# Optimization experiments

Measured on AMD Instinct MI355X. Metric: run time of the kernel, lower is better.

## Reference

```python
import jax, jax.numpy as jnp
import numpy as np

N_ATOMS = 16384
APC = 64            # atoms per conformer
N_CONF = 256        # 64 mols * 4 confs
N_MOL = 64
DEG = 32
E = N_ATOMS * DEG
H = 128             # hidden_channels = num_filters = out_channels
G = 50              # num_gaussians
L = 6               # num_interactions
CUTOFF = 10.0
LOG2 = float(np.log(2.0))


def ssp(x):
    # ShiftedSoftplus: softplus(x) - log(2)
    return jax.nn.softplus(x) - LOG2


def setup_inputs() -> dict:
    key = jax.random.key(0)
    ks = jax.random.split(key, 24)
    rng = np.random.default_rng(0)

    z = jnp.asarray(rng.integers(1, 100, size=(N_ATOMS,)), dtype=jnp.int64 if jax.config.jax_enable_x64 else jnp.int32)
    # positions uniform in a 5A box -> all intra-conformer distances < cutoff
    pos = jax.random.uniform(ks[0], (N_ATOMS, 3), dtype=jnp.float32) * 5.0

    # within-conformer random edges, no self loops (radius_graph surrogate)
    i = np.repeat(np.arange(N_ATOMS), DEG)
    off = rng.integers(1, APC, size=E)
    j = (i // APC) * APC + (i % APC + off) % APC
    edge_index = jnp.asarray(np.stack([j, i]), dtype=jnp.int32)  # [2,E] (source, target)

    atom_to_conf = jnp.asarray(np.arange(N_ATOMS) // APC, dtype=jnp.int32)
    conf_to_mol = jnp.asarray(np.arange(N_CONF) // (N_CONF // N_MOL), dtype=jnp.int32)

    s = 0.05
    p = {
        'emb':     jax.random.normal(ks[1], (120, H), jnp.float32) * s,
        # per-interaction stacked params [L, ...]
        'mlp_w1':  jax.random.normal(ks[2], (L, G, H), jnp.float32) * s,
        'mlp_b1':  jnp.zeros((L, H), jnp.float32),
        'mlp_w2':  jax.random.normal(ks[3], (L, H, H), jnp.float32) * s,
        'mlp_b2':  jnp.zeros((L, H), jnp.float32),
        'cf_w1':   jax.random.normal(ks[4], (L, H, H), jnp.float32) * s,
        'cf_w2':   jax.random.normal(ks[5], (L, H, H), jnp.float32) * s,
        'cf_b2':   jnp.zeros((L, H), jnp.float32),
        'int_w':   jax.random.normal(ks[6], (L, H, H), jnp.float32) * s,
        'int_b':   jnp.zeros((L, H), jnp.float32),
        # readout head
        'out_w1':  jax.random.normal(ks[7], (H, H), jnp.float32) * s,
        'out_b1':  jnp.zeros((H,), jnp.float32),
        'out_w2':  jax.random.normal(ks[8], (H, H), jnp.float32) * s,
        'out_b2':  jnp.zeros((H,), jnp.float32),
        'head_w1': jax.random.normal(ks[9], (H, H // 2), jnp.float32) * s,
        'head_b1': jnp.zeros((H // 2,), jnp.float32),
        'head_w2': jax.random.normal(ks[10], (H // 2, 1), jnp.float32) * s,
        'head_b2': jnp.zeros((1,), jnp.float32),
    }
    return dict(z=z, pos=pos, edge_index=edge_index, atom_to_conf=atom_to_conf,
                conf_to_mol=conf_to_mol, **p)


def reference(z, pos, edge_index, atom_to_conf, conf_to_mol, emb,
              mlp_w1, mlp_b1, mlp_w2, mlp_b2, cf_w1, cf_w2, cf_b2,
              int_w, int_b, out_w1, out_b1, out_w2, out_b2,
              head_w1, head_b1, head_w2, head_b2):
    row, col = edge_index[0], edge_index[1]  # message from row, aggregated at col

    h = emb[z]                                             # [N,H]
    edge_weight = jnp.linalg.norm(pos[row] - pos[col], axis=-1)  # [E]

    # GaussianSmearing
    offset = jnp.linspace(0.0, CUTOFF, G)
    coeff = -0.5 / (offset[1] - offset[0]) ** 2
    edge_attr = jnp.exp(coeff * (edge_weight[:, None] - offset[None, :]) ** 2)  # [E,G]

    C = 0.5 * (jnp.cos(edge_weight * jnp.pi / CUTOFF) + 1.0)  # cosine cutoff [E]

    for l in range(L):
        # filter network on edge features, modulated by cutoff envelope
        Wf = ssp(edge_attr @ mlp_w1[l] + mlp_b1[l]) @ mlp_w2[l] + mlp_b2[l]
        Wf = Wf * C[:, None]                               # [E,H]
        xf = h @ cf_w1[l]                                  # lin1 (no bias) [N,H]
        msg = xf[row] * Wf                                 # gather * filter [E,H]
        agg = jax.ops.segment_sum(msg, col, num_segments=N_ATOMS)  # scatter-add [N,H]
        xc = agg @ cf_w2[l] + cf_b2[l]                     # lin2
        h = h + (ssp(xc) @ int_w[l] + int_b[l])            # act, lin, residual

    h = ssp(h @ out_w1 + out_b1)
    h = h @ out_w2 + out_b2                                # [N,H]

    conf_emb = jax.ops.segment_sum(h, atom_to_conf, num_segments=N_CONF)   # [C,H]
    mol_emb = jax.ops.segment_sum(conf_emb, conf_to_mol, num_segments=N_MOL)  # [M,H]

    out = (ssp(mol_emb @ head_w1 + head_b1) @ head_w2 + head_b2)[:, 0]  # [M]
    return out
```

## Files before the change

### kernel.cpp

```cpp
#include <hip/hip_runtime.h>
#include <math.h>

#define N_ATOMS 16384
#define APC 64
#define N_CONF 256
#define N_MOL 64
#define DEG 32
#define NEDGE (N_ATOMS * DEG)
#define H 128
#define G 50
#define NL 6
#define TP0 1024
#define TPB 4096
#define CUTOFF 10.0f

typedef __attribute__((ext_vector_type(8))) short short8_t;
typedef __attribute__((ext_vector_type(4))) float f32x4;

__device__ __forceinline__ float ssp_f(float x) {
  float e = __expf(-fabsf(x));
  return fmaxf(x, 0.f) + __logf(1.f + e) - 0.69314718055994531f;
}
__device__ __forceinline__ unsigned short bf16_rne(float x) {
  unsigned u = __float_as_uint(x);
  unsigned r = u + 0x7FFF + ((u >> 16) & 1);
  return (unsigned short)(r >> 16);
}
__device__ __forceinline__ float bf16_to_f(unsigned short s) {
  return __uint_as_float(((unsigned)s) << 16);
}
__device__ __forceinline__ float bflo(unsigned u) { return __uint_as_float(u << 16); }
__device__ __forceinline__ float bfhi(unsigned u) { return __uint_as_float(u & 0xFFFF0000u); }

__global__ __launch_bounds__(256) void k_setup(
    const float* __restrict__ pos, const int* __restrict__ esrc,
    const int* __restrict__ etgt, int* __restrict__ pk,
    const float* __restrict__ cf_w1, const float* __restrict__ cf_w2,
    const float* __restrict__ int_w, const float* __restrict__ out_w1,
    const float* __restrict__ out_w2, short* __restrict__ PW,
    const float* __restrict__ w1, const float* __restrict__ b1,
    const float* __restrict__ w2, const float* __restrict__ b2,
    float* __restrict__ T) {
  __shared__ float g2[2][64];
  __shared__ float S2[2][128];
  const int b = blockIdx.x;
  const int tid = threadIdx.x;
  if (b < 2048) {
    int e = b * 256 + tid;
    int r = esrc[e], c = etgt[e];
    float dx = pos[r * 3 + 0] - pos[c * 3 + 0];
    float dy = pos[r * 3 + 1] - pos[c * 3 + 1];
    float dz = pos[r * 3 + 2] - pos[c * 3 + 2];
    float d = sqrtf(dx * dx + dy * dy + dz * dz);
    int i = (int)(d * ((float)(TPB - 1) / CUTOFF) + 0.5f);
    if (i > TPB - 1) i = TPB - 1;
    if (i < 0) i = 0;
    pk[e] = i | ((r & (APC - 1)) << 16);
  } else if (b < 2208) {
    int e = (b - 2048) * 256 + tid;
    int g = e >> 11, t = e & 2047;
    int kb = t >> 9, rem = t & 511, nt = rem >> 6, lane = rem & 63;
    int quad = lane >> 4, ln = lane & 15;
    int kbase = kb * 32 + quad * 8;
    int n = nt * 16 + ln;
    const float* src;
    if (g < 12) {
      int l = g >> 1;
      src = (g & 1) ? (int_w + l * 16384) : (cf_w2 + l * 16384);
    } else if (g < 18) {
      src = cf_w1 + (g - 12) * 16384;
    } else {
      src = (g == 18) ? out_w1 : out_w2;
    }
    short hv[8], lv[8];
    #pragma unroll
    for (int j = 0; j < 8; j++) {
      float x = src[(kbase + j) * H + n];
      unsigned short hb = bf16_rne(x);
      hv[j] = (short)hb;
      lv[j] = (short)bf16_rne(x - bf16_to_f(hb));
    }
    size_t base = (size_t)g * 32768 + (size_t)t * 8;
    *(short8_t*)&PW[base] = *(short8_t*)hv;
    *(short8_t*)&PW[base + 16384] = *(short8_t*)lv;
  } else {
    int bb = b - 2208;
    const int l = bb >> 9;
    const int grp = tid >> 7;
    const int c = tid & 127;
    const int p = (bb & 511) * 2 + grp;
    const float d = (float)p * (CUTOFF / (float)(TP0 - 1));
    const float gspace = CUTOFF / (float)(G - 1);
    const float coeff = -0.5f / (gspace * gspace);
    if (c < G) {
      float x = d - (float)c * gspace;
      g2[grp][c] = __expf(coeff * x * x);
    }
    __syncthreads();
    const float* W1 = w1 + l * G * H;
    float s = b1[l * H + c];
    #pragma unroll 5
    for (int i = 0; i < G; i++) s += g2[grp][i] * W1[i * H + c];
    S2[grp][c] = ssp_f(s);
    __syncthreads();
    const float* W2 = w2 + l * H * H;
    float o = b2[l * H + c];
    #pragma unroll 8
    for (int j = 0; j < H; j++) o += S2[grp][j] * W2[j * H + c];
    float Cc = 0.5f * (__cosf(d * (3.14159265358979f / CUTOFF)) + 1.f);
    T[((size_t)l * TP0 + p) * H + c] = o * Cc;
  }
}

__global__ __launch_bounds__(256) void k_up(const float* __restrict__ T,
                                            unsigned short* __restrict__ Tb) {
  int flat = blockIdx.x * 256 + threadIdx.x;
  int l = flat >> 19;
  int rem = flat & 524287;
  int p4 = rem >> 7, c = rem & 127;
  float u = (float)p4 * ((float)(TP0 - 1) / (float)(TPB - 1));
  int i = (int)u;
  if (i > TP0 - 2) i = TP0 - 2;
  float f = u - (float)i;
  const float* Tl = T + ((size_t)l * TP0 + i) * H + c;
  float v = Tl[0] + f * (Tl[H] - Tl[0]);
  Tb[flat] = bf16_rne(v);
}

#define MFMA(a, b, c) __builtin_amdgcn_mfma_f32_16x16x32_bf16((a), (b), (c), 0, 0, 0)

__device__ __forceinline__ void load_afrags(const short (*AH)[136], const short (*AL)[136],
                                            int rt, int ln, int quad,
                                            short8_t ah[4], short8_t al[4]) {
  #pragma unroll
  for (int kb = 0; kb < 4; kb++) {
    int ko = kb * 32 + quad * 8;
    ah[kb] = *(const short8_t*)&AH[rt * 16 + ln][ko];
    al[kb] = *(const short8_t*)&AL[rt * 16 + ln][ko];
  }
}

__device__ __forceinline__ void gemm2w(const short8_t ah[4], const short8_t al[4],
                                       const short* __restrict__ pw, int nt0, int lane,
                                       f32x4 acc[2]) {
  #pragma unroll
  for (int ct = 0; ct < 2; ct++) {
    int nt = nt0 + ct;
    f32x4 a = {0.f, 0.f, 0.f, 0.f};
    #pragma unroll
    for (int kb = 0; kb < 4; kb++) {
      const short* pb = pw + ((size_t)(kb * 8 + nt) * 64 + lane) * 8;
      short8_t bh = *(const short8_t*)pb;
      short8_t bl = *(const short8_t*)(pb + 16384);
      a = MFMA(ah[kb], bh, a);
      a = MFMA(ah[kb], bl, a);
      a = MFMA(al[kb], bh, a);
    }
    acc[ct] = a;
  }
}

__global__ __launch_bounds__(1024) void k_mega(
    const int* __restrict__ z, const float* __restrict__ emb,
    const int* __restrict__ pk, const unsigned short* __restrict__ Tb,
    const short* __restrict__ PW, const float* __restrict__ cf_b2,
    const float* __restrict__ int_b, const float* __restrict__ out_b1,
    const float* __restrict__ out_b2, float* __restrict__ conf_emb) {
  __shared__ float xs[64][132];
  __shared__ __align__(16) short hH[64][136], hL[64][136];
  __shared__ __align__(16) short S1H[64][136], S1L[64][136];
  __shared__ int pks[2048];
  __shared__ float ps[4][128];
  const int conf = blockIdx.x;
  const int tid = threadIdx.x;
  const int lane = tid & 63, w = tid >> 6;
  const int quad = lane >> 4, ln = lane & 15;
  const int rt = w & 3, nt0 = (w >> 2) * 2;
  const int eg = lane >> 4, ch0 = (lane & 15) * 8;

  pks[tid] = pk[conf * 2048 + tid];
  pks[tid + 1024] = pk[conf * 2048 + 1024 + tid];

  {
    int r = tid >> 4, cb = (tid & 15) * 8;
    const float* src = emb + (size_t)z[conf * 64 + r] * H + cb;
    float4 v0 = *(const float4*)src, v1 = *(const float4*)(src + 4);
    float vv[8] = {v0.x, v0.y, v0.z, v0.w, v1.x, v1.y, v1.z, v1.w};
    short hv[8], lv[8];
    #pragma unroll
    for (int u = 0; u < 8; u++) {
      unsigned short hb = bf16_rne(vv[u]);
      hv[u] = (short)hb;
      lv[u] = (short)bf16_rne(vv[u] - bf16_to_f(hb));
    }
    *(short8_t*)&hH[r][cb] = *(short8_t*)hv;
    *(short8_t*)&hL[r][cb] = *(short8_t*)lv;
  }
  __syncthreads();

  {
    short8_t ah[4], al_[4];
    load_afrags(hH, hL, rt, ln, quad, ah, al_);
    f32x4 acc[2];
    gemm2w(ah, al_, PW + (size_t)12 * 32768, nt0, lane, acc);
    #pragma unroll
    for (int ct = 0; ct < 2; ct++)
      #pragma unroll
      for (int reg = 0; reg < 4; reg++)
        xs[rt * 16 + quad * 4 + reg][(nt0 + ct) * 16 + ln] = acc[ct][reg];
  }
  __syncthreads();

  for (int l = 0; l < NL; l++) {
    const unsigned short* Tl = Tb + (size_t)l * TPB * H;
    #pragma unroll
    for (int aa = 0; aa < 4; aa++) {
      int a2 = w * 4 + aa;
      float acc[8] = {};
      #pragma unroll
      for (int it = 0; it < 8; it++) {
        int m = pks[a2 * DEG + it * 4 + eg];
        int idx = m & 0xFFFF, sl = m >> 16;
        uint4 tv = *(const uint4*)&Tl[(size_t)idx * H + ch0];
        float4 x0 = *(const float4*)&xs[sl][ch0];
        float4 x1 = *(const float4*)&xs[sl][ch0 + 4];
        acc[0] += bflo(tv.x) * x0.x; acc[1] += bfhi(tv.x) * x0.y;
        acc[2] += bflo(tv.y) * x0.z; acc[3] += bfhi(tv.y) * x0.w;
        acc[4] += bflo(tv.z) * x1.x; acc[5] += bfhi(tv.z) * x1.y;
        acc[6] += bflo(tv.w) * x1.z; acc[7] += bfhi(tv.w) * x1.w;
      }
      #pragma unroll
      for (int j = 0; j < 8; j++) {
        acc[j] += __shfl_xor(acc[j], 16);
        acc[j] += __shfl_xor(acc[j], 32);
      }
      if (eg == 0) {
        short hv[8], lv[8];
        #pragma unroll
        for (int j = 0; j < 8; j++) {
          unsigned short hb = bf16_rne(acc[j]);
          hv[j] = (short)hb;
          lv[j] = (short)bf16_rne(acc[j] - bf16_to_f(hb));
        }
        *(short8_t*)&S1H[a2][ch0] = *(short8_t*)hv;
        *(short8_t*)&S1L[a2][ch0] = *(short8_t*)lv;
      }
    }
    __syncthreads();
    {
      short8_t ah[4], al_[4];
      load_afrags(S1H, S1L, rt, ln, quad, ah, al_);
      f32x4 acc[2];
      gemm2w(ah, al_, PW + (size_t)(2 * l) * 32768, nt0, lane, acc);
      __syncthreads();
      #pragma unroll
      for (int ct = 0; ct < 2; ct++) {
        int col = (nt0 + ct) * 16 + ln;
        float bb = cf_b2[l * H + col];
        #pragma unroll
        for (int reg = 0; reg < 4; reg++) {
          int row = rt * 16 + quad * 4 + reg;
          float v = ssp_f(acc[ct][reg] + bb);
          unsigned short hb = bf16_rne(v);
          S1H[row][col] = (short)hb;
          S1L[row][col] = (short)bf16_rne(v - bf16_to_f(hb));
        }
      }
    }
    __syncthreads();
    {
      short8_t ah[4], al_[4];
      load_afrags(S1H, S1L, rt, ln, quad, ah, al_);
      f32x4 acc[2];
      gemm2w(ah, al_, PW + (size_t)(2 * l + 1) * 32768, nt0, lane, acc);
      #pragma unroll
      for (int ct = 0; ct < 2; ct++) {
        int col = (nt0 + ct) * 16 + ln;
        float bb = int_b[l * H + col];
        #pragma unroll
        for (int reg = 0; reg < 4; reg++) {
          int row = rt * 16 + quad * 4 + reg;
          float hv = bf16_to_f((unsigned short)hH[row][col]) +
                     bf16_to_f((unsigned short)hL[row][col]);
          float v = acc[ct][reg] + bb + hv;
          unsigned short hb = bf16_rne(v);
          hH[row][col] = (short)hb;
          hL[row][col] = (short)bf16_rne(v - bf16_to_f(hb));
        }
      }
    }
    __syncthreads();
    if (l < NL - 1) {
      short8_t ah[4], al_[4];
      load_afrags(hH, hL, rt, ln, quad, ah, al_);
      f32x4 acc[2];
      gemm2w(ah, al_, PW + (size_t)(13 + l) * 32768, nt0, lane, acc);
      #pragma unroll
      for (int ct = 0; ct < 2; ct++)
        #pragma unroll
        for (int reg = 0; reg < 4; reg++)
          xs[rt * 16 + quad * 4 + reg][(nt0 + ct) * 16 + ln] = acc[ct][reg];
      __syncthreads();
    }
  }

  {
    short8_t ah[4], al_[4];
    load_afrags(hH, hL, rt, ln, quad, ah, al_);
    f32x4 acc[2];
    gemm2w(ah, al_, PW + (size_t)18 * 32768, nt0, lane, acc);
    __syncthreads();
    #pragma unroll
    for (int ct = 0; ct < 2; ct++) {
      int col = (nt0 + ct) * 16 + ln;
      float bb = out_b1[col];
      #pragma unroll
      for (int reg = 0; reg < 4; reg++) {
        int row = rt * 16 + quad * 4 + reg;
        float v = ssp_f(acc[ct][reg] + bb);
        unsigned short hb = bf16_rne(v);
        S1H[row][col] = (short)hb;
        S1L[row][col] = (short)bf16_rne(v - bf16_to_f(hb));
      }
    }
  }
  __syncthreads();
  {
    short8_t ah[4], al_[4];
    load_afrags(S1H, S1L, rt, ln, quad, ah, al_);
    f32x4 acc[2];
    gemm2w(ah, al_, PW + (size_t)19 * 32768, nt0, lane, acc);
    #pragma unroll
    for (int ct = 0; ct < 2; ct++) {
      int col = (nt0 + ct) * 16 + ln;
      float s = acc[ct][0] + acc[ct][1] + acc[ct][2] + acc[ct][3] + 4.f * out_b2[col];
      s += __shfl_xor(s, 16);
      s += __shfl_xor(s, 32);
      if (quad == 0) ps[rt][col] = s;
    }
  }
  __syncthreads();
  if (tid < 128) {
    conf_emb[conf * 128 + tid] =
        ps[0][tid] + ps[1][tid] + ps[2][tid] + ps[3][tid];
  }
}

__global__ __launch_bounds__(128) void k_pool_head(const float* __restrict__ ce,
                                                   const float* __restrict__ hw1,
                                                   const float* __restrict__ hb1,
                                                   const float* __restrict__ hw2,
                                                   const float* __restrict__ hb2,
                                                   float* __restrict__ outp) {
  int m = blockIdx.x;
  int c = threadIdx.x;
  __shared__ float mol[128];
  __shared__ float q[64];
  const float* base = ce + (size_t)m * 4 * H;
  mol[c] = base[c] + base[H + c] + base[2 * H + c] + base[3 * H + c];
  __syncthreads();
  if (c < 64) {
    float qq = hb1[c];
    #pragma unroll 8
    for (int cc = 0; cc < H; cc++) qq += mol[cc] * hw1[cc * 64 + c];
    q[c] = ssp_f(qq);
  }
  __syncthreads();
  if (c == 0) {
    float o = hb2[0];
    for (int j = 0; j < 64; j++) o += q[j] * hw2[j];
    outp[m] = o;
  }
}

extern "C" void kernel_launch(void* const* d_in, const int* in_sizes, int n_in,
                              void* d_out, int out_size, void* d_ws, size_t ws_size,
                              hipStream_t stream) {
  const int*   z       = (const int*)d_in[0];
  const float* pos     = (const float*)d_in[1];
  const int*   eidx    = (const int*)d_in[2];
  const float* emb     = (const float*)d_in[5];
  const float* mlp_w1  = (const float*)d_in[6];
  const float* mlp_b1  = (const float*)d_in[7];
  const float* mlp_w2  = (const float*)d_in[8];
  const float* mlp_b2  = (const float*)d_in[9];
  const float* cf_w1   = (const float*)d_in[10];
  const float* cf_w2   = (const float*)d_in[11];
  const float* cf_b2   = (const float*)d_in[12];
  const float* int_w   = (const float*)d_in[13];
  const float* int_b   = (const float*)d_in[14];
  const float* out_w1  = (const float*)d_in[15];
  const float* out_b1  = (const float*)d_in[16];
  const float* out_w2  = (const float*)d_in[17];
  const float* out_b2  = (const float*)d_in[18];
  const float* head_w1 = (const float*)d_in[19];
  const float* head_b1 = (const float*)d_in[20];
  const float* head_w2 = (const float*)d_in[21];
  const float* head_b2 = (const float*)d_in[22];

  float* ws = (float*)d_ws;
  float*          T    = ws;
  unsigned short* Tb   = (unsigned short*)(T + 786432);
  int*            pk   = (int*)(Tb + 3145728);
  short*          PW   = (short*)(pk + 524288);
  float*          ce   = (float*)(PW + 655360);

  k_setup<<<5280, 256, 0, stream>>>(pos, eidx, eidx + NEDGE, pk,
                                    cf_w1, cf_w2, int_w, out_w1, out_w2, PW,
                                    mlp_w1, mlp_b1, mlp_w2, mlp_b2, T);
  k_up<<<(NL * TPB * H) / 256, 256, 0, stream>>>(T, Tb);

  k_mega<<<N_CONF, 1024, 0, stream>>>(z, emb, pk, Tb, PW, cf_b2, int_b,
                                      out_b1, out_b2, ce);

  k_pool_head<<<N_MOL, 128, 0, stream>>>(ce, head_w1, head_b1, head_w2, head_b2,
                                         (float*)d_out);
}
```

Baseline: 255.0 us.

## Fuse pooling head into mega kernel, halve filter table, restructure GEMM tiling

Several changes at once. The coarse filter table is halved (TP0 1024→512), so k_setup does less work. k_up is vectorised to process four channels per thread. In k_mega the MFMA tiling changes so each wave covers two row tiles for one column tile, reusing the B fragments. Separate tH/tL buffers remove a sync. The gather loop preloads byte-offset table entries before the FMAs and uses packed f32x2 FMAs. The k_pool_head launch is removed; the last block to finish, found with an atomic counter, computes the head. Risks are coarser interpolation accuracy, more LDS use, and a serial tail in the last block.

```diff
diff --git a/kernel.cpp b/kernel.cpp
--- a/kernel.cpp
+++ b/kernel.cpp
@@ -10,12 +10,13 @@
 #define H 128
 #define G 50
 #define NL 6
-#define TP0 1024
+#define TP0 512
 #define TPB 4096
 #define CUTOFF 10.0f
 
 typedef __attribute__((ext_vector_type(8))) short short8_t;
 typedef __attribute__((ext_vector_type(4))) float f32x4;
+typedef __attribute__((ext_vector_type(2))) float f32x2;
 
 __device__ __forceinline__ float ssp_f(float x) {
   float e = __expf(-fabsf(x));
@@ -40,11 +41,12 @@
     const float* __restrict__ out_w2, short* __restrict__ PW,
     const float* __restrict__ w1, const float* __restrict__ b1,
     const float* __restrict__ w2, const float* __restrict__ b2,
-    float* __restrict__ T) {
+    float* __restrict__ T, int* __restrict__ cnt) {
   __shared__ float g2[2][64];
   __shared__ float S2[2][128];
   const int b = blockIdx.x;
   const int tid = threadIdx.x;
+  if (b == 0 && tid == 0) *cnt = 0;
   if (b < 2048) {
     int e = b * 256 + tid;
     int r = esrc[e], c = etgt[e];
@@ -55,7 +57,7 @@
     int i = (int)(d * ((float)(TPB - 1) / CUTOFF) + 0.5f);
     if (i > TPB - 1) i = TPB - 1;
     if (i < 0) i = 0;
-    pk[e] = i | ((r & (APC - 1)) << 16);
+    pk[e] = (i << 8) | ((r & (APC - 1)) << 20);
   } else if (b < 2208) {
     int e = (b - 2048) * 256 + tid;
     int g = e >> 11, t = e & 2047;
@@ -85,10 +87,10 @@
     *(short8_t*)&PW[base + 16384] = *(short8_t*)lv;
   } else {
     int bb = b - 2208;
-    const int l = bb >> 9;
+    const int l = bb >> 8;
     const int grp = tid >> 7;
     const int c = tid & 127;
-    const int p = (bb & 511) * 2 + grp;
+    const int p = (bb & 255) * 2 + grp;
     const float d = (float)p * (CUTOFF / (float)(TP0 - 1));
     const float gspace = CUTOFF / (float)(G - 1);
     const float coeff = -0.5f / (gspace * gspace);
@@ -114,68 +116,71 @@
 
 __global__ __launch_bounds__(256) void k_up(const float* __restrict__ T,
                                             unsigned short* __restrict__ Tb) {
-  int flat = blockIdx.x * 256 + threadIdx.x;
-  int l = flat >> 19;
-  int rem = flat & 524287;
-  int p4 = rem >> 7, c = rem & 127;
+  int t = blockIdx.x * 256 + threadIdx.x;
+  int l = t >> 17;
+  int rem = t & 131071;
+  int p4 = rem >> 5, cg = rem & 31;
+  int c = cg * 4;
   float u = (float)p4 * ((float)(TP0 - 1) / (float)(TPB - 1));
   int i = (int)u;
   if (i > TP0 - 2) i = TP0 - 2;
   float f = u - (float)i;
-  const float* Tl = T + ((size_t)l * TP0 + i) * H + c;
-  float v = Tl[0] + f * (Tl[H] - Tl[0]);
-  Tb[flat] = bf16_rne(v);
+  const float* a = T + ((size_t)l * TP0 + i) * H + c;
+  float4 v0 = *(const float4*)a;
+  float4 v1 = *(const float4*)(a + H);
+  ushort4 o;
+  o.x = bf16_rne(v0.x + f * (v1.x - v0.x));
+  o.y = bf16_rne(v0.y + f * (v1.y - v0.y));
+  o.z = bf16_rne(v0.z + f * (v1.z - v0.z));
+  o.w = bf16_rne(v0.w + f * (v1.w - v0.w));
+  *(ushort4*)&Tb[((size_t)l * TPB + p4) * H + c] = o;
 }
 
 #define MFMA(a, b, c) __builtin_amdgcn_mfma_f32_16x16x32_bf16((a), (b), (c), 0, 0, 0)
 
-__device__ __forceinline__ void load_afrags(const short (*AH)[136], const short (*AL)[136],
-                                            int rt, int ln, int quad,
-                                            short8_t ah[4], short8_t al[4]) {
+__device__ __forceinline__ void gemm_rt2(const short (*AH)[136], const short (*AL)[136],
+                                         const short* __restrict__ pw,
+                                         int rt2, int nt, int lane, int quad, int ln,
+                                         f32x4 acc[2]) {
   #pragma unroll
   for (int kb = 0; kb < 4; kb++) {
+    const short* pb = pw + ((size_t)(kb * 8 + nt) * 64 + lane) * 8;
+    short8_t bh = *(const short8_t*)pb;
+    short8_t bl = *(const short8_t*)(pb + 16384);
     int ko = kb * 32 + quad * 8;
-    ah[kb] = *(const short8_t*)&AH[rt * 16 + ln][ko];
-    al[kb] = *(const short8_t*)&AL[rt * 16 + ln][ko];
-  }
-}
-
-__device__ __forceinline__ void gemm2w(const short8_t ah[4], const short8_t al[4],
-                                       const short* __restrict__ pw, int nt0, int lane,
-                                       f32x4 acc[2]) {
-  #pragma unroll
-  for (int ct = 0; ct < 2; ct++) {
-    int nt = nt0 + ct;
-    f32x4 a = {0.f, 0.f, 0.f, 0.f};
     #pragma unroll
-    for (int kb = 0; kb < 4; kb++) {
-      const short* pb = pw + ((size_t)(kb * 8 + nt) * 64 + lane) * 8;
-      short8_t bh = *(const short8_t*)pb;
-      short8_t bl = *(const short8_t*)(pb + 16384);
-      a = MFMA(ah[kb], bh, a);
-      a = MFMA(ah[kb], bl, a);
-      a = MFMA(al[kb], bh, a);
-    }
-    acc[ct] = a;
-  }
-}
-
-__global__ __launch_bounds__(1024) void k_mega(
+    for (int rtt = 0; rtt < 2; rtt++) {
+      int row = rt2 * 32 + rtt * 16 + ln;
+      short8_t ah = *(const short8_t*)&AH[row][ko];
+      short8_t al = *(const short8_t*)&AL[row][ko];
+      acc[rtt] = MFMA(ah, bh, acc[rtt]);
+      acc[rtt] = MFMA(ah, bl, acc[rtt]);
+      acc[rtt] = MFMA(al, bh, acc[rtt]);
+    }
+  }
+}
+
+__global__ __launch_bounds__(1024, 1) void k_mega(
     const int* __restrict__ z, const float* __restrict__ emb,
     const int* __restrict__ pk, const unsigned short* __restrict__ Tb,
     const short* __restrict__ PW, const float* __restrict__ cf_b2,
     const float* __restrict__ int_b, const float* __restrict__ out_b1,
-    const float* __restrict__ out_b2, float* __restrict__ conf_emb) {
+    const float* __restrict__ out_b2, float* __restrict__ ce,
+    const float* __restrict__ hw1, const float* __restrict__ hb1,
+    const float* __restrict__ hw2, const float* __restrict__ hb2,
+    int* __restrict__ cnt, float* __restrict__ outp) {
   __shared__ float xs[64][132];
   __shared__ __align__(16) short hH[64][136], hL[64][136];
+  __shared__ __align__(16) short tH[64][136], tL[64][136];
   __shared__ __align__(16) short S1H[64][136], S1L[64][136];
   __shared__ int pks[2048];
-  __shared__ float ps[4][128];
+  __shared__ float ps[2][128];
+  __shared__ int is_last;
   const int conf = blockIdx.x;
   const int tid = threadIdx.x;
   const int lane = tid & 63, w = tid >> 6;
   const int quad = lane >> 4, ln = lane & 15;
-  const int rt = w & 3, nt0 = (w >> 2) * 2;
+  const int rt2 = w & 1, nt = w >> 1;
   const int eg = lane >> 4, ch0 = (lane & 15) * 8;
 
   pks[tid] = pk[conf * 2048 + tid];
@@ -199,177 +204,180 @@
   __syncthreads();
 
   {
-    short8_t ah[4], al_[4];
-    load_afrags(hH, hL, rt, ln, quad, ah, al_);
-    f32x4 acc[2];
-    gemm2w(ah, al_, PW + (size_t)12 * 32768, nt0, lane, acc);
+    f32x4 acc[2] = {{0.f, 0.f, 0.f, 0.f}, {0.f, 0.f, 0.f, 0.f}};
+    gemm_rt2(hH, hL, PW + (size_t)12 * 32768, rt2, nt, lane, quad, ln, acc);
+    int col = nt * 16 + ln;
     #pragma unroll
-    for (int ct = 0; ct < 2; ct++)
+    for (int rtt = 0; rtt < 2; rtt++)
       #pragma unroll
       for (int reg = 0; reg < 4; reg++)
-        xs[rt * 16 + quad * 4 + reg][(nt0 + ct) * 16 + ln] = acc[ct][reg];
+        xs[rt2 * 32 + rtt * 16 + quad * 4 + reg][col] = acc[rtt][reg];
   }
   __syncthreads();
 
   for (int l = 0; l < NL; l++) {
-    const unsigned short* Tl = Tb + (size_t)l * TPB * H;
-    #pragma unroll
+    const char* Tlb = (const char*)(Tb + (size_t)l * TPB * H) + ch0 * 2;
+    #pragma unroll 1
     for (int aa = 0; aa < 4; aa++) {
       int a2 = w * 4 + aa;
-      float acc[8] = {};
+      int ms[8];
+      uint4 tvv[8];
       #pragma unroll
       for (int it = 0; it < 8; it++) {
-        int m = pks[a2 * DEG + it * 4 + eg];
-        int idx = m & 0xFFFF, sl = m >> 16;
-        uint4 tv = *(const uint4*)&Tl[(size_t)idx * H + ch0];
-        float4 x0 = *(const float4*)&xs[sl][ch0];
-        float4 x1 = *(const float4*)&xs[sl][ch0 + 4];
-        acc[0] += bflo(tv.x) * x0.x; acc[1] += bfhi(tv.x) * x0.y;
-        acc[2] += bflo(tv.y) * x0.z; acc[3] += bfhi(tv.y) * x0.w;
-        acc[4] += bflo(tv.z) * x1.x; acc[5] += bfhi(tv.z) * x1.y;
-        acc[6] += bflo(tv.w) * x1.z; acc[7] += bfhi(tv.w) * x1.w;
+        ms[it] = pks[a2 * DEG + it * 4 + eg];
+        tvv[it] = *(const uint4*)(Tlb + (ms[it] & 0xFFFFF));
       }
+      f32x2 ac0 = {0.f, 0.f}, ac1 = {0.f, 0.f}, ac2 = {0.f, 0.f}, ac3 = {0.f, 0.f};
+      #pragma unroll
+      for (int it = 0; it < 8; it++) {
+        int sl = ms[it] >> 20;
+        const float* xr = &xs[sl][ch0];
+        float4 x0 = *(const float4*)xr;
+        float4 x1 = *(const float4*)(xr + 4);
+        uint4 tv = tvv[it];
+        ac0 = __builtin_elementwise_fma((f32x2){bflo(tv.x), bfhi(tv.x)},
+                                        (f32x2){x0.x, x0.y}, ac0);
+        ac1 = __builtin_elementwise_fma((f32x2){bflo(tv.y), bfhi(tv.y)},
+                                        (f32x2){x0.z, x0.w}, ac1);
+        ac2 = __builtin_elementwise_fma((f32x2){bflo(tv.z), bfhi(tv.z)},
+                                        (f32x2){x1.x, x1.y}, ac2);
+        ac3 = __builtin_elementwise_fma((f32x2){bflo(tv.w), bfhi(tv.w)},
+                                        (f32x2){x1.z, x1.w}, ac3);
+      }
+      float accs[8] = {ac0.x, ac0.y, ac1.x, ac1.y, ac2.x, ac2.y, ac3.x, ac3.y};
       #pragma unroll
       for (int j = 0; j < 8; j++) {
-        acc[j] += __shfl_xor(acc[j], 16);
-        acc[j] += __shfl_xor(acc[j], 32);
+        accs[j] += __shfl_xor(accs[j], 16);
+        accs[j] += __shfl_xor(accs[j], 32);
       }
-      if (eg == 0) {
-        short hv[8], lv[8];
-        #pragma unroll
-        for (int j = 0; j < 8; j++) {
-          unsigned short hb = bf16_rne(acc[j]);
-          hv[j] = (short)hb;
-          lv[j] = (short)bf16_rne(acc[j] - bf16_to_f(hb));
-        }
-        *(short8_t*)&S1H[a2][ch0] = *(short8_t*)hv;
-        *(short8_t*)&S1L[a2][ch0] = *(short8_t*)lv;
-      }
+      float va = eg == 0 ? accs[0] : eg == 1 ? accs[2] : eg == 2 ? accs[4] : accs[6];
+      float vb = eg == 0 ? accs[1] : eg == 1 ? accs[3] : eg == 2 ? accs[5] : accs[7];
+      unsigned short ha = bf16_rne(va), hb = bf16_rne(vb);
+      unsigned short la = bf16_rne(va - bf16_to_f(ha));
+      unsigned short lb = bf16_rne(vb - bf16_to_f(hb));
+      int cw = ch0 + eg * 2;
+      *(short2*)&S1H[a2][cw] = make_short2((short)ha, (short)hb);
+      *(short2*)&S1L[a2][cw] = make_short2((short)la, (short)lb);
     }
     __syncthreads();
     {
-      short8_t ah[4], al_[4];
-      load_afrags(S1H, S1L, rt, ln, quad, ah, al_);
-      f32x4 acc[2];
-      gemm2w(ah, al_, PW + (size_t)(2 * l) * 32768, nt0, lane, acc);
-      __syncthreads();
-      #pragma unroll
-      for (int ct = 0; ct < 2; ct++) {
-        int col = (nt0 + ct) * 16 + ln;
-        float bb = cf_b2[l * H + col];
+      f32x4 acc[2] = {{0.f, 0.f, 0.f, 0.f}, {0.f, 0.f, 0.f, 0.f}};
+      gemm_rt2(S1H, S1L, PW + (size_t)(2 * l) * 32768, rt2, nt, lane, quad, ln, acc);
+      int col = nt * 16 + ln;
+      float bb = cf_b2[l * H + col];
+      #pragma unroll
+      for (int rtt = 0; rtt < 2; rtt++)
         #pragma unroll
         for (int reg = 0; reg < 4; reg++) {
-          int row = rt * 16 + quad * 4 + reg;
-          float v = ssp_f(acc[ct][reg] + bb);
+          int row = rt2 * 32 + rtt * 16 + quad * 4 + reg;
+          float v = ssp_f(acc[rtt][reg] + bb);
           unsigned short hb = bf16_rne(v);
-          S1H[row][col] = (short)hb;
-          S1L[row][col] = (short)bf16_rne(v - bf16_to_f(hb));
+          tH[row][col] = (short)hb;
+          tL[row][col] = (short)bf16_rne(v - bf16_to_f(hb));
         }
-      }
     }
     __syncthreads();
     {
-      short8_t ah[4], al_[4];
-      load_afrags(S1H, S1L, rt, ln, quad, ah, al_);
-      f32x4 acc[2];
-      gemm2w(ah, al_, PW + (size_t)(2 * l + 1) * 32768, nt0, lane, acc);
-      #pragma unroll
-      for (int ct = 0; ct < 2; ct++) {
-        int col = (nt0 + ct) * 16 + ln;
-        float bb = int_b[l * H + col];
+      f32x4 acc[2] = {{0.f, 0.f, 0.f, 0.f}, {0.f, 0.f, 0.f, 0.f}};
+      gemm_rt2(tH, tL, PW + (size_t)(2 * l + 1) * 32768, rt2, nt, lane, quad, ln, acc);
+      int col = nt * 16 + ln;
+      float bb = int_b[l * H + col];
+      #pragma unroll
+      for (int rtt = 0; rtt < 2; rtt++)
         #pragma unroll
         for (int reg = 0; reg < 4; reg++) {
-          int row = rt * 16 + quad * 4 + reg;
+          int row = rt2 * 32 + rtt * 16 + quad * 4 + reg;
           float hv = bf16_to_f((unsigned short)hH[row][col]) +
                      bf16_to_f((unsigned short)hL[row][col]);
-          float v = acc[ct][reg] + bb + hv;
+          float v = acc[rtt][reg] + bb + hv;
           unsigned short hb = bf16_rne(v);
           hH[row][col] = (short)hb;
           hL[row][col] = (short)bf16_rne(v - bf16_to_f(hb));
         }
-      }
     }
     __syncthreads();
     if (l < NL - 1) {
-      short8_t ah[4], al_[4];
-      load_afrags(hH, hL, rt, ln, quad, ah, al_);
-      f32x4 acc[2];
-      gemm2w(ah, al_, PW + (size_t)(13 + l) * 32768, nt0, lane, acc);
-      #pragma unroll
-      for (int ct = 0; ct < 2; ct++)
+      f32x4 acc[2] = {{0.f, 0.f, 0.f, 0.f}, {0.f, 0.f, 0.f, 0.f}};
+      gemm_rt2(hH, hL, PW + (size_t)(13 + l) * 32768, rt2, nt, lane, quad, ln, acc);
+      int col = nt * 16 + ln;
+      #pragma unroll
+      for (int rtt = 0; rtt < 2; rtt++)
         #pragma unroll
         for (int reg = 0; reg < 4; reg++)
-          xs[rt * 16 + quad * 4 + reg][(nt0 + ct) * 16 + ln] = acc[ct][reg];
+          xs[rt2 * 32 + rtt * 16 + quad * 4 + reg][col] = acc[rtt][reg];
       __syncthreads();
     }
   }
 
   {
-    short8_t ah[4], al_[4];
-    load_afrags(hH, hL, rt, ln, quad, ah, al_);
-    f32x4 acc[2];
-    gemm2w(ah, al_, PW + (size_t)18 * 32768, nt0, lane, acc);
-    __syncthreads();
+    f32x4 acc[2] = {{0.f, 0.f, 0.f, 0.f}, {0.f, 0.f, 0.f, 0.f}};
+    gemm_rt2(hH, hL, PW + (size_t)18 * 32768, rt2, nt, lane, quad, ln, acc);
+    int col = nt * 16 + ln;
+    float bb = out_b1[col];
     #pragma unroll
-    for (int ct = 0; ct < 2; ct++) {
-      int col = (nt0 + ct) * 16 + ln;
-      float bb = out_b1[col];
+    for (int rtt = 0; rtt < 2; rtt++)
       #pragma unroll
       for (int reg = 0; reg < 4; reg++) {
-        int row = rt * 16 + quad * 4 + reg;
-        float v = ssp_f(acc[ct][reg] + bb);
+        int row = rt2 * 32 + rtt * 16 + quad * 4 + reg;
+        float v = ssp_f(acc[rtt][reg] + bb);
         unsigned short hb = bf16_rne(v);
-        S1H[row][col] = (short)hb;
-        S1L[row][col] = (short)bf16_rne(v - bf16_to_f(hb));
+        tH[row][col] = (short)hb;
+        tL[row][col] = (short)bf16_rne(v - bf16_to_f(hb));
       }
-    }
   }
   __syncthreads();
   {
-    short8_t ah[4], al_[4];
-    load_afrags(S1H, S1L, rt, ln, quad, ah, al_);
-    f32x4 acc[2];
-    gemm2w(ah, al_, PW + (size_t)19 * 32768, nt0, lane, acc);
-    #pragma unroll
-    for (int ct = 0; ct < 2; ct++) {
-      int col = (nt0 + ct) * 16 + ln;
-      float s = acc[ct][0] + acc[ct][1] + acc[ct][2] + acc[ct][3] + 4.f * out_b2[col];
-      s += __shfl_xor(s, 16);
-      s += __shfl_xor(s, 32);
-      if (quad == 0) ps[rt][col] = s;
-    }
+    f32x4 acc[2] = {{0.f, 0.f, 0.f, 0.f}, {0.f, 0.f, 0.f, 0.f}};
+    gemm_rt2(tH, tL, PW + (size_t)19 * 32768, rt2, nt, lane, quad, ln, acc);
+    int col = nt * 16 + ln;
+    float s = acc[0][0] + acc[0][1] + acc[0][2] + acc[0][3] +
+              acc[1][0] + acc[1][1] + acc[1][2] + acc[1][3];
+    s += __shfl_xor(s, 16);
+    s += __shfl_xor(s, 32);
+    if (quad == 0) ps[rt2][col] = s;
   }
   __syncthreads();
   if (tid < 128) {
-    conf_emb[conf * 128 + tid] =
-        ps[0][tid] + ps[1][tid] + ps[2][tid] + ps[3][tid];
-  }
-}
-
-__global__ __launch_bounds__(128) void k_pool_head(const float* __restrict__ ce,
-                                                   const float* __restrict__ hw1,
-                                                   const float* __restrict__ hb1,
-                                                   const float* __restrict__ hw2,
-                                                   const float* __restrict__ hb2,
-                                                   float* __restrict__ outp) {
-  int m = blockIdx.x;
-  int c = threadIdx.x;
-  __shared__ float mol[128];
-  __shared__ float q[64];
-  const float* base = ce + (size_t)m * 4 * H;
-  mol[c] = base[c] + base[H + c] + base[2 * H + c] + base[3 * H + c];
-  __syncthreads();
-  if (c < 64) {
-    float qq = hb1[c];
-    #pragma unroll 8
-    for (int cc = 0; cc < H; cc++) qq += mol[cc] * hw1[cc * 64 + c];
-    q[c] = ssp_f(qq);
-  }
-  __syncthreads();
-  if (c == 0) {
-    float o = hb2[0];
-    for (int j = 0; j < 64; j++) o += q[j] * hw2[j];
-    outp[m] = o;
+    float v = ps[0][tid] + ps[1][tid] + 64.f * out_b2[tid];
+    __hip_atomic_store(&ce[conf * 128 + tid], v, __ATOMIC_RELAXED,
+                       __HIP_MEMORY_SCOPE_AGENT);
+  }
+  __syncthreads();
+  if (tid == 0) {
+    __threadfence();
+    int old = __hip_atomic_fetch_add(cnt, 1, __ATOMIC_ACQ_REL,
+                                     __HIP_MEMORY_SCOPE_AGENT);
+    is_last = (old == N_CONF - 1) ? 1 : 0;
+  }
+  __syncthreads();
+  if (is_last) {
+    __threadfence();
+    float* mol = &xs[0][0];
+    for (int t = tid; t < N_MOL * 128; t += 1024) {
+      int m = t >> 7, c = t & 127;
+      const float* b = ce + (size_t)(m * 4) * 128;
+      float s = __hip_atomic_load(&b[c], __ATOMIC_RELAXED, __HIP_MEMORY_SCOPE_AGENT) +
+                __hip_atomic_load(&b[128 + c], __ATOMIC_RELAXED, __HIP_MEMORY_SCOPE_AGENT) +
+                __hip_atomic_load(&b[256 + c], __ATOMIC_RELAXED, __HIP_MEMORY_SCOPE_AGENT) +
+                __hip_atomic_load(&b[384 + c], __ATOMIC_RELAXED, __HIP_MEMORY_SCOPE_AGENT);
+      mol[t] = s;
+    }
+    __syncthreads();
+    float* q = (float*)&S1H[0][0];
+    for (int t = tid; t < N_MOL * 64; t += 1024) {
+      int m = t >> 6, j = t & 63;
+      float qq = hb1[j];
+      #pragma unroll 8
+      for (int c = 0; c < H; c++) qq += mol[m * 128 + c] * hw1[c * 64 + j];
+      q[t] = ssp_f(qq);
+    }
+    __syncthreads();
+    if (tid < N_MOL) {
+      float o = hb2[0];
+      #pragma unroll 8
+      for (int j = 0; j < 64; j++) o += q[tid * 64 + j] * hw2[j];
+      outp[tid] = o;
+    }
   }
 }
 
@@ -398,21 +406,22 @@
   const float* head_w2 = (const float*)d_in[21];
   const float* head_b2 = (const float*)d_in[22];
 
-  float* ws = (float*)d_ws;
-  float*          T    = ws;
-  unsigned short* Tb   = (unsigned short*)(T + 786432);
-  int*            pk   = (int*)(Tb + 3145728);
-  short*          PW   = (short*)(pk + 524288);
-  float*          ce   = (float*)(PW + 655360);
-
-  k_setup<<<5280, 256, 0, stream>>>(pos, eidx, eidx + NEDGE, pk,
+  char* ws = (char*)d_ws;
+  float*          T   = (float*)ws;
+  unsigned short* Tb  = (unsigned short*)(ws + (size_t)NL * TP0 * H * 4);
+  char*           p2  = (char*)Tb + (size_t)NL * TPB * H * 2;
+  int*            pk  = (int*)p2;
+  short*          PW  = (short*)(p2 + (size_t)NEDGE * 4);
+  float*          ce  = (float*)((char*)PW + (size_t)20 * 32768 * 2);
+  int*            cnt = (int*)((char*)ce + (size_t)N_CONF * H * 4);
+
+  k_setup<<<3744, 256, 0, stream>>>(pos, eidx, eidx + NEDGE, pk,
                                     cf_w1, cf_w2, int_w, out_w1, out_w2, PW,
-                                    mlp_w1, mlp_b1, mlp_w2, mlp_b2, T);
-  k_up<<<(NL * TPB * H) / 256, 256, 0, stream>>>(T, Tb);
+                                    mlp_w1, mlp_b1, mlp_w2, mlp_b2, T, cnt);
+  k_up<<<(NL * TPB * H / 4) / 256, 256, 0, stream>>>(T, Tb);
 
   k_mega<<<N_CONF, 1024, 0, stream>>>(z, emb, pk, Tb, PW, cf_b2, int_b,
-                                      out_b1, out_b2, ce);
-
-  k_pool_head<<<N_MOL, 128, 0, stream>>>(ce, head_w1, head_b1, head_w2, head_b2,
-                                         (float*)d_out);
-}
+                                      out_b1, out_b2, ce,
+                                      head_w1, head_b1, head_w2, head_b2,
+                                      cnt, (float*)d_out);
+}
```

Result: faster. 243.1 us (-4.7%).

## Fuse edge-distance prep and pooling head into mega kernel, halve filter table

Applied to the files above, without the earlier changes.

Moves the per-edge distance and table-index computation into the main per-conformer kernel using positions staged in shared memory, so the separate pk buffer round trip goes away. It also fuses the molecule pooling and head MLP into the last finishing block through an atomic counter, which removes one kernel launch. The coarse filter table is halved from 1024 to 512 points, cutting setup MLP work, and the upsampling kernel is vectorised to process four channels per thread. Risks are coarser interpolation accuracy, a serial tail in the last block, and a memset added to each launch for the counter.

```diff
diff --git a/kernel.cpp b/kernel.cpp
--- a/kernel.cpp
+++ b/kernel.cpp
@@ -10,7 +10,7 @@
 #define H 128
 #define G 50
 #define NL 6
-#define TP0 1024
+#define TP0 512
 #define TPB 4096
 #define CUTOFF 10.0f
 
@@ -33,8 +33,6 @@
 __device__ __forceinline__ float bfhi(unsigned u) { return __uint_as_float(u & 0xFFFF0000u); }
 
 __global__ __launch_bounds__(256) void k_setup(
-    const float* __restrict__ pos, const int* __restrict__ esrc,
-    const int* __restrict__ etgt, int* __restrict__ pk,
     const float* __restrict__ cf_w1, const float* __restrict__ cf_w2,
     const float* __restrict__ int_w, const float* __restrict__ out_w1,
     const float* __restrict__ out_w2, short* __restrict__ PW,
@@ -45,19 +43,8 @@
   __shared__ float S2[2][128];
   const int b = blockIdx.x;
   const int tid = threadIdx.x;
-  if (b < 2048) {
+  if (b < 160) {
     int e = b * 256 + tid;
-    int r = esrc[e], c = etgt[e];
-    float dx = pos[r * 3 + 0] - pos[c * 3 + 0];
-    float dy = pos[r * 3 + 1] - pos[c * 3 + 1];
-    float dz = pos[r * 3 + 2] - pos[c * 3 + 2];
-    float d = sqrtf(dx * dx + dy * dy + dz * dz);
-    int i = (int)(d * ((float)(TPB - 1) / CUTOFF) + 0.5f);
-    if (i > TPB - 1) i = TPB - 1;
-    if (i < 0) i = 0;
-    pk[e] = i | ((r & (APC - 1)) << 16);
-  } else if (b < 2208) {
-    int e = (b - 2048) * 256 + tid;
     int g = e >> 11, t = e & 2047;
     int kb = t >> 9, rem = t & 511, nt = rem >> 6, lane = rem & 63;
     int quad = lane >> 4, ln = lane & 15;
@@ -84,11 +71,11 @@
     *(short8_t*)&PW[base] = *(short8_t*)hv;
     *(short8_t*)&PW[base + 16384] = *(short8_t*)lv;
   } else {
-    int bb = b - 2208;
-    const int l = bb >> 9;
+    int bb = b - 160;
+    const int l = bb >> 8;
     const int grp = tid >> 7;
     const int c = tid & 127;
-    const int p = (bb & 511) * 2 + grp;
+    const int p = (bb & 255) * 2 + grp;
     const float d = (float)p * (CUTOFF / (float)(TP0 - 1));
     const float gspace = CUTOFF / (float)(G - 1);
     const float coeff = -0.5f / (gspace * gspace);
@@ -114,17 +101,24 @@
 
 __global__ __launch_bounds__(256) void k_up(const float* __restrict__ T,
                                             unsigned short* __restrict__ Tb) {
-  int flat = blockIdx.x * 256 + threadIdx.x;
-  int l = flat >> 19;
-  int rem = flat & 524287;
-  int p4 = rem >> 7, c = rem & 127;
+  int t = blockIdx.x * 256 + threadIdx.x;
+  int l = t >> 17;
+  int rem = t & 131071;
+  int p4 = rem >> 5, cg = rem & 31;
+  int c = cg * 4;
   float u = (float)p4 * ((float)(TP0 - 1) / (float)(TPB - 1));
   int i = (int)u;
   if (i > TP0 - 2) i = TP0 - 2;
   float f = u - (float)i;
-  const float* Tl = T + ((size_t)l * TP0 + i) * H + c;
-  float v = Tl[0] + f * (Tl[H] - Tl[0]);
-  Tb[flat] = bf16_rne(v);
+  const float* a = T + ((size_t)l * TP0 + i) * H + c;
+  float4 v0 = *(const float4*)a;
+  float4 v1 = *(const float4*)(a + H);
+  ushort4 o;
+  o.x = bf16_rne(v0.x + f * (v1.x - v0.x));
+  o.y = bf16_rne(v0.y + f * (v1.y - v0.y));
+  o.z = bf16_rne(v0.z + f * (v1.z - v0.z));
+  o.w = bf16_rne(v0.w + f * (v1.w - v0.w));
+  *(ushort4*)&Tb[((size_t)l * TPB + p4) * H + c] = o;
 }
 
 #define MFMA(a, b, c) __builtin_amdgcn_mfma_f32_16x16x32_bf16((a), (b), (c), 0, 0, 0)
@@ -160,17 +154,23 @@
   }
 }
 
-__global__ __launch_bounds__(1024) void k_mega(
-    const int* __restrict__ z, const float* __restrict__ emb,
-    const int* __restrict__ pk, const unsigned short* __restrict__ Tb,
-    const short* __restrict__ PW, const float* __restrict__ cf_b2,
-    const float* __restrict__ int_b, const float* __restrict__ out_b1,
-    const float* __restrict__ out_b2, float* __restrict__ conf_emb) {
+__global__ __launch_bounds__(1024, 1) void k_mega(
+    const int* __restrict__ z, const float* __restrict__ pos,
+    const int* __restrict__ esrc, const float* __restrict__ emb,
+    const unsigned short* __restrict__ Tb, const short* __restrict__ PW,
+    const float* __restrict__ cf_b2, const float* __restrict__ int_b,
+    const float* __restrict__ out_b1, const float* __restrict__ out_b2,
+    float* __restrict__ ce, const float* __restrict__ hw1,
+    const float* __restrict__ hb1, const float* __restrict__ hw2,
+    const float* __restrict__ hb2, int* __restrict__ cnt,
+    float* __restrict__ outp) {
   __shared__ float xs[64][132];
   __shared__ __align__(16) short hH[64][136], hL[64][136];
   __shared__ __align__(16) short S1H[64][136], S1L[64][136];
   __shared__ int pks[2048];
   __shared__ float ps[4][128];
+  __shared__ float posL[192];
+  __shared__ int is_last;
   const int conf = blockIdx.x;
   const int tid = threadIdx.x;
   const int lane = tid & 63, w = tid >> 6;
@@ -178,9 +178,23 @@
   const int rt = w & 3, nt0 = (w >> 2) * 2;
   const int eg = lane >> 4, ch0 = (lane & 15) * 8;
 
-  pks[tid] = pk[conf * 2048 + tid];
-  pks[tid + 1024] = pk[conf * 2048 + 1024 + tid];
-
+  if (tid < 192) posL[tid] = pos[conf * 192 + tid];
+  __syncthreads();
+  #pragma unroll
+  for (int k = 0; k < 2; k++) {
+    int e2 = k * 1024 + tid;
+    int r = esrc[conf * 2048 + e2];
+    int rl = r & (APC - 1);
+    int ca = e2 >> 5;
+    float dx = posL[rl * 3 + 0] - posL[ca * 3 + 0];
+    float dy = posL[rl * 3 + 1] - posL[ca * 3 + 1];
+    float dz = posL[rl * 3 + 2] - posL[ca * 3 + 2];
+    float d = sqrtf(dx * dx + dy * dy + dz * dz);
+    int i = (int)(d * ((float)(TPB - 1) / CUTOFF) + 0.5f);
+    if (i > TPB - 1) i = TPB - 1;
+    if (i < 0) i = 0;
+    pks[e2] = i | (rl << 16);
+  }
   {
     int r = tid >> 4, cb = (tid & 15) * 8;
     const float* src = emb + (size_t)z[conf * 64 + r] * H + cb;
@@ -333,7 +347,7 @@
     #pragma unroll
     for (int ct = 0; ct < 2; ct++) {
       int col = (nt0 + ct) * 16 + ln;
-      float s = acc[ct][0] + acc[ct][1] + acc[ct][2] + acc[ct][3] + 4.f * out_b2[col];
+      float s = acc[ct][0] + acc[ct][1] + acc[ct][2] + acc[ct][3];
       s += __shfl_xor(s, 16);
       s += __shfl_xor(s, 32);
       if (quad == 0) ps[rt][col] = s;
@@ -341,35 +355,46 @@
   }
   __syncthreads();
   if (tid < 128) {
-    conf_emb[conf * 128 + tid] =
-        ps[0][tid] + ps[1][tid] + ps[2][tid] + ps[3][tid];
-  }
-}
-
-__global__ __launch_bounds__(128) void k_pool_head(const float* __restrict__ ce,
-                                                   const float* __restrict__ hw1,
-                                                   const float* __restrict__ hb1,
-                                                   const float* __restrict__ hw2,
-                                                   const float* __restrict__ hb2,
-                                                   float* __restrict__ outp) {
-  int m = blockIdx.x;
-  int c = threadIdx.x;
-  __shared__ float mol[128];
-  __shared__ float q[64];
-  const float* base = ce + (size_t)m * 4 * H;
-  mol[c] = base[c] + base[H + c] + base[2 * H + c] + base[3 * H + c];
-  __syncthreads();
-  if (c < 64) {
-    float qq = hb1[c];
-    #pragma unroll 8
-    for (int cc = 0; cc < H; cc++) qq += mol[cc] * hw1[cc * 64 + c];
-    q[c] = ssp_f(qq);
-  }
-  __syncthreads();
-  if (c == 0) {
-    float o = hb2[0];
-    for (int j = 0; j < 64; j++) o += q[j] * hw2[j];
-    outp[m] = o;
+    float v = ps[0][tid] + ps[1][tid] + ps[2][tid] + ps[3][tid] + 64.f * out_b2[tid];
+    __hip_atomic_store(&ce[conf * 128 + tid], v, __ATOMIC_RELAXED,
+                       __HIP_MEMORY_SCOPE_AGENT);
+  }
+  __syncthreads();
+  if (tid == 0) {
+    __threadfence();
+    int old = __hip_atomic_fetch_add(cnt, 1, __ATOMIC_ACQ_REL,
+                                     __HIP_MEMORY_SCOPE_AGENT);
+    is_last = (old == N_CONF - 1) ? 1 : 0;
+  }
+  __syncthreads();
+  if (is_last) {
+    __threadfence();
+    float* mol = &xs[0][0];
+    for (int t = tid; t < N_MOL * 128; t += 1024) {
+      int m = t >> 7, c = t & 127;
+      const float* bb = ce + (size_t)(m * 4) * 128;
+      float s = __hip_atomic_load(&bb[c], __ATOMIC_RELAXED, __HIP_MEMORY_SCOPE_AGENT) +
+                __hip_atomic_load(&bb[128 + c], __ATOMIC_RELAXED, __HIP_MEMORY_SCOPE_AGENT) +
+                __hip_atomic_load(&bb[256 + c], __ATOMIC_RELAXED, __HIP_MEMORY_SCOPE_AGENT) +
+                __hip_atomic_load(&bb[384 + c], __ATOMIC_RELAXED, __HIP_MEMORY_SCOPE_AGENT);
+      mol[t] = s;
+    }
+    __syncthreads();
+    float* q = (float*)&S1H[0][0];
+    for (int t = tid; t < N_MOL * 64; t += 1024) {
+      int m = t >> 6, j = t & 63;
+      float qq = hb1[j];
+      #pragma unroll 8
+      for (int c = 0; c < H; c++) qq += mol[m * 128 + c] * hw1[c * 64 + j];
+      q[t] = ssp_f(qq);
+    }
+    __syncthreads();
+    if (tid < N_MOL) {
+      float o = hb2[0];
+      #pragma unroll 8
+      for (int j = 0; j < 64; j++) o += q[tid * 64 + j] * hw2[j];
+      outp[tid] = o;
+    }
   }
 }
 
@@ -398,21 +423,19 @@
   const float* head_w2 = (const float*)d_in[21];
   const float* head_b2 = (const float*)d_in[22];
 
-  float* ws = (float*)d_ws;
-  float*          T    = ws;
-  unsigned short* Tb   = (unsigned short*)(T + 786432);
-  int*            pk   = (int*)(Tb + 3145728);
-  short*          PW   = (short*)(pk + 524288);
-  float*          ce   = (float*)(PW + 655360);
-
-  k_setup<<<5280, 256, 0, stream>>>(pos, eidx, eidx + NEDGE, pk,
-                                    cf_w1, cf_w2, int_w, out_w1, out_w2, PW,
+  char* ws = (char*)d_ws;
+  float*          T   = (float*)ws;
+  unsigned short* Tb  = (unsigned short*)(ws + 1572864);
+  short*          PW  = (short*)(ws + 1572864 + 6291456);
+  float*          ce  = (float*)(ws + 9175040);
+  int*            cnt = (int*)(ws + 9306112);
+
+  hipMemsetAsync(cnt, 0, 4, stream);
+  k_setup<<<1696, 256, 0, stream>>>(cf_w1, cf_w2, int_w, out_w1, out_w2, PW,
                                     mlp_w1, mlp_b1, mlp_w2, mlp_b2, T);
-  k_up<<<(NL * TPB * H) / 256, 256, 0, stream>>>(T, Tb);
-
-  k_mega<<<N_CONF, 1024, 0, stream>>>(z, emb, pk, Tb, PW, cf_b2, int_b,
-                                      out_b1, out_b2, ce);
-
-  k_pool_head<<<N_MOL, 128, 0, stream>>>(ce, head_w1, head_b1, head_w2, head_b2,
-                                         (float*)d_out);
-}
+  k_up<<<(NL * TPB * H / 4) / 256, 256, 0, stream>>>(T, Tb);
+  k_mega<<<N_CONF, 1024, 0, stream>>>(z, pos, eidx, emb, Tb, PW, cf_b2, int_b,
+                                      out_b1, out_b2, ce,
+                                      head_w1, head_b1, head_w2, head_b2,
+                                      cnt, (float*)d_out);
+}
```

Result: slower. 271.8 us (+6.6%).
